# Performance work log

Measured on AMD Instinct MI355X. Metric: run time of the kernel, lower is better.

Reference implementation:

```python
import jax, jax.numpy as jnp
import numpy as np

EPS = 1e-5
QB = 128.0  # 2**(bit-1), bit=8

def _int8_wrap(q):
    # Emulate torch's .to(torch.int8) two's-complement wrap (e.g. 128 -> -128).
    return jnp.mod(q + 128.0, 256.0) - 128.0

def setup_inputs() -> dict:
    key = jax.random.key(0)
    k1, k2, k3 = jax.random.split(key, 3)
    x = jax.random.normal(k1, (4, 2048, 2048), dtype=jnp.float32)
    weights = jax.random.normal(k2, (8192, 2048), dtype=jnp.float32)
    bias = jax.random.normal(k3, (8192,), dtype=jnp.float32)
    return {"x": x, "weights": weights, "bias": bias}

def reference(x, weights, bias):
    in_features = x.shape[-1]
    out_features = weights.shape[0]
    # LayerNorm over last dim, no affine (F.layer_norm defaults, eps=1e-5)
    mu = jnp.mean(x, axis=-1, keepdims=True)
    var = jnp.mean(jnp.square(x - mu), axis=-1, keepdims=True)
    input_norm = (x - mu) * jax.lax.rsqrt(var + EPS)
    # absmax int8 activation quant (nl_next=False path)
    max_val = jnp.max(jnp.abs(input_norm))
    q = _int8_wrap(jnp.round(input_norm * (QB / max_val)))
    dequant = max_val / QB
    # weight sign-binarization around the mean
    weight_quant = jnp.sign(weights - jnp.mean(weights))
    # quantized matmul + dequant scales + bias
    out = jnp.einsum('bsd,od->bso', q, weight_quant)  # [B,S,out]
    beta = jnp.sum(jnp.abs(weights)) / (in_features * out_features)
    out = out * (dequant * beta) + bias
    return out
```

## Files before the change

### kernel.cpp

```cpp
#include <hip/hip_runtime.h>


using i32x4 = __attribute__((ext_vector_type(4))) int;

typedef const __attribute__((address_space(1))) void cg_void;
typedef __attribute__((address_space(3))) void lds_void;

#define K_DIM 2048
#define N_DIM 8192
#define M_DIM 8192
#define NELEM_W 16777216


__global__ __launch_bounds__(256) void pass1(const float* __restrict__ x,
                                             const float4* __restrict__ w4,
                                             float* __restrict__ mu_arr,
                                             float* __restrict__ rstd_arr,
                                             float* __restrict__ rowmax,
                                             double2* __restrict__ part) {
    __shared__ double sbd[8];
    __shared__ float sb1[4];
    __shared__ float sb2[8];
    const int bid = blockIdx.x, t = threadIdx.x;
    const int lane = t & 63, wv = t >> 6;
    if (bid < 1024) {
        double s = 0.0, a = 0.0;
        for (int i = bid * 256 + t; i < NELEM_W / 4; i += 1024 * 256) {
            float4 v = w4[i];
            s += (double)v.x + (double)v.y + (double)v.z + (double)v.w;
            a += fabs((double)v.x) + fabs((double)v.y) + fabs((double)v.z) + fabs((double)v.w);
        }
        for (int o = 32; o; o >>= 1) { s += __shfl_xor(s, o); a += __shfl_xor(a, o); }
        if (lane == 0) { sbd[wv] = s; sbd[4 + wv] = a; }
        __syncthreads();
        if (t == 0) {
            double2 r;
            r.x = sbd[0] + sbd[1] + sbd[2] + sbd[3];
            r.y = sbd[4] + sbd[5] + sbd[6] + sbd[7];
            part[bid] = r;
        }
    } else {
        const int row = bid - 1024;
        const float4* xr = (const float4*)x + (size_t)row * 512;
        float4 v0 = xr[t], v1 = xr[t + 256];
        float s = v0.x + v0.y + v0.z + v0.w + v1.x + v1.y + v1.z + v1.w;
        for (int o = 32; o; o >>= 1) s += __shfl_xor(s, o);
        if (lane == 0) sb1[wv] = s;
        __syncthreads();
        float mu = (sb1[0] + sb1[1] + sb1[2] + sb1[3]) * (1.0f / 2048.0f);
        float ssq = 0.f, md = 0.f, d;
        d = v0.x - mu; ssq += d * d; md = fmaxf(md, fabsf(d));
        d = v0.y - mu; ssq += d * d; md = fmaxf(md, fabsf(d));
        d = v0.z - mu; ssq += d * d; md = fmaxf(md, fabsf(d));
        d = v0.w - mu; ssq += d * d; md = fmaxf(md, fabsf(d));
        d = v1.x - mu; ssq += d * d; md = fmaxf(md, fabsf(d));
        d = v1.y - mu; ssq += d * d; md = fmaxf(md, fabsf(d));
        d = v1.z - mu; ssq += d * d; md = fmaxf(md, fabsf(d));
        d = v1.w - mu; ssq += d * d; md = fmaxf(md, fabsf(d));
        for (int o = 32; o; o >>= 1) {
            ssq += __shfl_xor(ssq, o);
            md = fmaxf(md, __shfl_xor(md, o));
        }
        if (lane == 0) { sb2[wv] = ssq; sb2[4 + wv] = md; }
        __syncthreads();
        if (t == 0) {
            float var = (sb2[0] + sb2[1] + sb2[2] + sb2[3]) * (1.0f / 2048.0f);
            float rstd = 1.0f / sqrtf(var + 1e-5f);
            mu_arr[row] = mu;
            rstd_arr[row] = rstd;
            rowmax[row] = fmaxf(fmaxf(sb2[4], sb2[5]), fmaxf(sb2[6], sb2[7])) * rstd;
        }
    }
}

__global__ __launch_bounds__(256) void wred2(const double2* __restrict__ part,
                                             const float* __restrict__ rowmax,
                                             unsigned* __restrict__ scal) {
    double s = 0.0, a = 0.0;
    float m = 0.f;
    const int t = threadIdx.x, lane = t & 63, wv = t >> 6;
    for (int i = t; i < 1024; i += 256) { double2 p = part[i]; s += p.x; a += p.y; }
    for (int i = t; i < 8192; i += 256) m = fmaxf(m, rowmax[i]);
    for (int o = 32; o; o >>= 1) {
        s += __shfl_xor(s, o); a += __shfl_xor(a, o);
        m = fmaxf(m, __shfl_xor(m, o));
    }
    __shared__ double sbd[8];
    __shared__ float sbm[4];
    if (lane == 0) { sbd[wv] = s; sbd[4 + wv] = a; sbm[wv] = m; }
    __syncthreads();
    if (t == 0) {
        double st = sbd[0] + sbd[1] + sbd[2] + sbd[3];
        double at = sbd[4] + sbd[5] + sbd[6] + sbd[7];
        ((float*)scal)[0] = fmaxf(fmaxf(sbm[0], sbm[1]), fmaxf(sbm[2], sbm[3]));
        ((float*)scal)[1] = (float)(st / (double)NELEM_W);
        ((float*)scal)[2] = (float)(at / (double)NELEM_W);
    }
}

__device__ __forceinline__ int sgn8(float d) { return (d > 0.f) ? 1 : ((d < 0.f) ? -1 : 0); }

__global__ __launch_bounds__(256) void pass2(const float* __restrict__ x,
                                             const float4* __restrict__ w4,
                                             const float* __restrict__ mu_arr,
                                             const float* __restrict__ rstd_arr,
                                             const unsigned* __restrict__ scal,
                                             signed char* __restrict__ q,
                                             int4* __restrict__ wq4) {
    const int bid = blockIdx.x, t = threadIdx.x;
    if (bid < 1024) {
        float wm = ((const float*)scal)[1];
        for (int i = bid * 256 + t; i < NELEM_W / 16; i += 1024 * 256) {
            int words[4];
            #pragma unroll
            for (int jj = 0; jj < 4; ++jj) {
                float4 v = w4[i * 4 + jj];
                int b0 = sgn8(v.x - wm) & 255, b1 = sgn8(v.y - wm) & 255;
                int b2 = sgn8(v.z - wm) & 255, b3 = sgn8(v.w - wm) & 255;
                words[jj] = b0 | (b1 << 8) | (b2 << 16) | (b3 << 24);
            }
            wq4[i] = make_int4(words[0], words[1], words[2], words[3]);
        }
    } else {
        const int row = bid - 1024;
        float mu = mu_arr[row], rstd = rstd_arr[row];
        float s = 128.0f / ((const float*)scal)[0];
        const float4* xr = (const float4*)x + (size_t)row * 512;
        float4 v0 = xr[2 * t], v1 = xr[2 * t + 1];
        float xs[8] = {v0.x, v0.y, v0.z, v0.w, v1.x, v1.y, v1.z, v1.w};
        int b[8];
        #pragma unroll
        for (int j = 0; j < 8; ++j) {
            float norm = (xs[j] - mu) * rstd;
            int qi = (int)rintf(norm * s);
            b[j] = qi & 255;
        }
        int w0 = b[0] | (b[1] << 8) | (b[2] << 16) | (b[3] << 24);
        int w1 = b[4] | (b[5] << 8) | (b[6] << 16) | (b[7] << 24);
        ((int2*)(q + (size_t)row * 2048))[t] = make_int2(w0, w1);
    }
}

#define LD16(p) (*(const i32x4*)(p))

#define STAGE(aoff, boff, sbase)                                                            \
    do {                                                                                    \
        _Pragma("unroll") for (int i_ = 0; i_ < 4; ++i_)                                    \
            __builtin_amdgcn_global_load_lds((cg_void*)(gA + (size_t)i_ * 131072 + (aoff)), \
                (lds_void*)(lds + (sbase) + i_ * 8192 + w * 1024), 16, 0, 0);               \
        _Pragma("unroll") for (int i_ = 0; i_ < 4; ++i_)                                    \
            __builtin_amdgcn_global_load_lds((cg_void*)(gB + (size_t)i_ * 131072 + (boff)), \
                (lds_void*)(lds + (sbase) + 32768 + i_ * 8192 + w * 1024), 16, 0, 0);       \
    } while (0)

#define MF16(MB, BF)                                                                        \
    _Pragma("unroll") for (int mm = 0; mm < 4; ++mm)                                        \
        _Pragma("unroll") for (int nn = 0; nn < 4; ++nn)                                    \
            acc[(MB) + mm][nn] = __builtin_amdgcn_mfma_i32_16x16x64_i8(                     \
                af[mm], BF[nn], acc[(MB) + mm][nn], 0, 0, 0);

__global__ __launch_bounds__(512, 2) void gemm_i8(const signed char* __restrict__ A,
                                                  const signed char* __restrict__ B,
                                                  const float* __restrict__ bias,
                                                  const unsigned* __restrict__ scal,
                                                  float* __restrict__ C) {
    __shared__ alignas(16) char lds[131072];
    const int t = threadIdx.x, w = t >> 6, lane = t & 63;

    const int wg = blockIdx.x;
    const int xcd = wg & 7, j = wg >> 3;
    const int bm = (xcd * 4 + (j >> 3)) * 256;
    const int col0 = (j & 7) * 4;

    const int wr = w >> 2, wc = w & 3;
    const int r16 = lane & 15, ko = lane >> 4;

    const int srow = w * 8 + (lane >> 3);
    const int scol = ((lane & 7) ^ (lane >> 3)) << 4;
    const signed char* gA = A + (size_t)(bm + srow) * K_DIM + scol;
    const signed char* gB = B + (size_t)(col0 * 256 + srow) * K_DIM + scol;

    const char* aBase = lds + (wr * 128 + r16) * 128;
    const char* bBase = lds + 32768 + (wc * 64 + r16) * 128;
    const int xr = (r16 & 7) << 4;
    const int sw0 = (ko * 16) ^ xr;
    const int sw1 = (64 + ko * 16) ^ xr;

    const float scale = (((const float*)scal)[0] * (1.0f / 128.0f)) * ((const float*)scal)[2];

    i32x4 acc[8][4] = {};
    i32x4 af[4], bf0[4], bf1[4];

    STAGE(0, 0, 0);

    #pragma unroll 2
    for (int gt = 0; gt < 64; ++gt) {
        const int c = (gt & 1) << 16;
        if (gt < 63) {
            const int nt = gt + 1;
            const int kt1 = nt & 15, rep1 = nt >> 4;
            const size_t aoff = (size_t)(kt1 * 128);
            const size_t boff = (size_t)rep1 * 524288 + (size_t)(kt1 * 128);
            STAGE(aoff, boff, (nt & 1) << 16);
            asm volatile("s_waitcnt vmcnt(8)" ::: "memory");
        } else {
            asm volatile("s_waitcnt vmcnt(0)" ::: "memory");
        }
        __builtin_amdgcn_s_barrier();
        #pragma unroll
        for (int m = 0; m < 4; ++m) af[m] = LD16(aBase + c + m * 2048 + sw0);
        #pragma unroll
        for (int n = 0; n < 4; ++n) bf0[n] = LD16(bBase + c + n * 2048 + sw0);
        asm volatile("s_waitcnt lgkmcnt(0)" ::: "memory");
        __builtin_amdgcn_s_setprio(1);
        MF16(0, bf0);
        __builtin_amdgcn_s_setprio(0);
        __builtin_amdgcn_s_barrier();
        #pragma unroll
        for (int m = 0; m < 4; ++m) af[m] = LD16(aBase + c + m * 2048 + sw1);
        #pragma unroll
        for (int n = 0; n < 4; ++n) bf1[n] = LD16(bBase + c + n * 2048 + sw1);
        __builtin_amdgcn_s_barrier();
        asm volatile("s_waitcnt lgkmcnt(0)" ::: "memory");
        __builtin_amdgcn_s_setprio(1);
        MF16(0, bf1);
        __builtin_amdgcn_s_setprio(0);
        __builtin_amdgcn_s_barrier();
        #pragma unroll
        for (int m = 0; m < 4; ++m) af[m] = LD16(aBase + c + (4 + m) * 2048 + sw0);
        __builtin_amdgcn_s_barrier();
        asm volatile("s_waitcnt lgkmcnt(0)" ::: "memory");
        __builtin_amdgcn_s_setprio(1);
        MF16(4, bf0);
        __builtin_amdgcn_s_setprio(0);
        __builtin_amdgcn_s_barrier();
        #pragma unroll
        for (int m = 0; m < 4; ++m) af[m] = LD16(aBase + c + (4 + m) * 2048 + sw1);
        __builtin_amdgcn_s_barrier();
        asm volatile("s_waitcnt lgkmcnt(0)" ::: "memory");
        __builtin_amdgcn_s_setprio(1);
        MF16(4, bf1);
        __builtin_amdgcn_s_setprio(0);
        __builtin_amdgcn_s_barrier();

        if ((gt & 15) == 15) {
            const int rep = gt >> 4;
            const int colbase = (col0 + rep) * 256 + wc * 64;
            float bi[4];
            #pragma unroll
            for (int n = 0; n < 4; ++n) bi[n] = bias[colbase + n * 16 + r16];
            #pragma unroll
            for (int m = 0; m < 8; ++m) {
                #pragma unroll
                for (int n = 0; n < 4; ++n) {
                    #pragma unroll
                    for (int r = 0; r < 4; ++r) {
                        int row = bm + wr * 128 + m * 16 + ko * 4 + r;
                        int col = colbase + n * 16 + r16;
                        C[(size_t)row * N_DIM + col] = (float)acc[m][n][r] * scale + bi[n];
                    }
                }
            }
            #pragma unroll
            for (int m = 0; m < 8; ++m)
                #pragma unroll
                for (int n = 0; n < 4; ++n) acc[m][n] = (i32x4){0, 0, 0, 0};
        }
    }
}

extern "C" void kernel_launch(void* const* d_in, const int* in_sizes, int n_in,
                              void* d_out, int out_size, void* d_ws, size_t ws_size,
                              hipStream_t stream) {
    const float* x = (const float*)d_in[0];
    const float* wts = (const float*)d_in[1];
    const float* bias = (const float*)d_in[2];
    float* out = (float*)d_out;

    char* ws = (char*)d_ws;
    unsigned* scal = (unsigned*)ws;
    double2* part = (double2*)(ws + 1024);
    float* mu = (float*)(ws + 32768);
    float* rstd = (float*)(ws + 65536);
    float* rowmax = (float*)(ws + 98304);
    signed char* q = (signed char*)(ws + 131072);
    signed char* wq = (signed char*)(ws + 131072 + 16777216);

    hipLaunchKernelGGL(pass1, dim3(9216), dim3(256), 0, stream,
                       x, (const float4*)wts, mu, rstd, rowmax, part);
    hipLaunchKernelGGL(wred2, dim3(1), dim3(256), 0, stream, part, rowmax, scal);
    hipLaunchKernelGGL(pass2, dim3(9216), dim3(256), 0, stream,
                       x, (const float4*)wts, mu, rstd, scal, q, (int4*)wq);
    hipLaunchKernelGGL(gemm_i8, dim3(256), dim3(512), 0, stream,
                       q, wq, bias, scal, out);
}
```

Measured before the change: 244.3 us.

## Double-buffer A fragments and drop intra-tile barriers in int8 GEMM loop

Keeps two sets of A-fragment registers so LDS reads for the next MFMA block are issued before the current block runs. The explicit lgkmcnt waits and most per-phase barriers are removed, leaving only the barriers around the k-tile, so waves desynchronize and LDS latency can hide behind MFMAs. This uses more VGPRs, which may pressure the 2-waves-per-SIMD launch bound, and the compiler now decides where the waits go.

Measured after the change: 253.4 us. 1.04x slower.

```diff
diff --git a/kernel.cpp b/kernel.cpp
--- a/kernel.cpp
+++ b/kernel.cpp
@@ -153,11 +153,13 @@
                 (lds_void*)(lds + (sbase) + 32768 + i_ * 8192 + w * 1024), 16, 0, 0);       \
     } while (0)
 
-#define MF16(MB, BF)                                                                        \
+#define MFC(MB, AF, BF)                                                                     \
+    __builtin_amdgcn_s_setprio(1);                                                          \
     _Pragma("unroll") for (int mm = 0; mm < 4; ++mm)                                        \
         _Pragma("unroll") for (int nn = 0; nn < 4; ++nn)                                    \
             acc[(MB) + mm][nn] = __builtin_amdgcn_mfma_i32_16x16x64_i8(                     \
-                af[mm], BF[nn], acc[(MB) + mm][nn], 0, 0, 0);
+                AF[mm], BF[nn], acc[(MB) + mm][nn], 0, 0, 0);                               \
+    __builtin_amdgcn_s_setprio(0);
 
 __global__ __launch_bounds__(512, 2) void gemm_i8(const signed char* __restrict__ A,
                                                   const signed char* __restrict__ B,
@@ -189,7 +191,7 @@
     const float scale = (((const float*)scal)[0] * (1.0f / 128.0f)) * ((const float*)scal)[2];
 
     i32x4 acc[8][4] = {};
-    i32x4 af[4], bf0[4], bf1[4];
+    i32x4 a0[4], a1[4], b0[4], b1[4];
 
     STAGE(0, 0, 0);
 
@@ -207,40 +209,23 @@
             asm volatile("s_waitcnt vmcnt(0)" ::: "memory");
         }
         __builtin_amdgcn_s_barrier();
-        #pragma unroll
-        for (int m = 0; m < 4; ++m) af[m] = LD16(aBase + c + m * 2048 + sw0);
-        #pragma unroll
-        for (int n = 0; n < 4; ++n) bf0[n] = LD16(bBase + c + n * 2048 + sw0);
-        asm volatile("s_waitcnt lgkmcnt(0)" ::: "memory");
-        __builtin_amdgcn_s_setprio(1);
-        MF16(0, bf0);
-        __builtin_amdgcn_s_setprio(0);
-        __builtin_amdgcn_s_barrier();
-        #pragma unroll
-        for (int m = 0; m < 4; ++m) af[m] = LD16(aBase + c + m * 2048 + sw1);
-        #pragma unroll
-        for (int n = 0; n < 4; ++n) bf1[n] = LD16(bBase + c + n * 2048 + sw1);
-        __builtin_amdgcn_s_barrier();
-        asm volatile("s_waitcnt lgkmcnt(0)" ::: "memory");
-        __builtin_amdgcn_s_setprio(1);
-        MF16(0, bf1);
-        __builtin_amdgcn_s_setprio(0);
-        __builtin_amdgcn_s_barrier();
-        #pragma unroll
-        for (int m = 0; m < 4; ++m) af[m] = LD16(aBase + c + (4 + m) * 2048 + sw0);
-        __builtin_amdgcn_s_barrier();
-        asm volatile("s_waitcnt lgkmcnt(0)" ::: "memory");
-        __builtin_amdgcn_s_setprio(1);
-        MF16(4, bf0);
-        __builtin_amdgcn_s_setprio(0);
-        __builtin_amdgcn_s_barrier();
-        #pragma unroll
-        for (int m = 0; m < 4; ++m) af[m] = LD16(aBase + c + (4 + m) * 2048 + sw1);
-        __builtin_amdgcn_s_barrier();
-        asm volatile("s_waitcnt lgkmcnt(0)" ::: "memory");
-        __builtin_amdgcn_s_setprio(1);
-        MF16(4, bf1);
-        __builtin_amdgcn_s_setprio(0);
+
+        #pragma unroll
+        for (int m = 0; m < 4; ++m) a0[m] = LD16(aBase + c + m * 2048 + sw0);
+        #pragma unroll
+        for (int n = 0; n < 4; ++n) b0[n] = LD16(bBase + c + n * 2048 + sw0);
+        #pragma unroll
+        for (int m = 0; m < 4; ++m) a1[m] = LD16(aBase + c + (4 + m) * 2048 + sw0);
+        MFC(0, a0, b0);
+        #pragma unroll
+        for (int m = 0; m < 4; ++m) a0[m] = LD16(aBase + c + m * 2048 + sw1);
+        #pragma unroll
+        for (int n = 0; n < 4; ++n) b1[n] = LD16(bBase + c + n * 2048 + sw1);
+        MFC(4, a1, b0);
+        #pragma unroll
+        for (int m = 0; m < 4; ++m) a1[m] = LD16(aBase + c + (4 + m) * 2048 + sw1);
+        MFC(0, a0, b1);
+        MFC(4, a1, b1);
         __builtin_amdgcn_s_barrier();
 
         if ((gt & 15) == 15) {
```
